# Performance work log

Hardware: AMD Instinct MI355X
Metric: run time of the kernel (lower is better)

The kernel has to match this reference:

```python
import jax, jax.numpy as jnp
import numpy as np

EOS_COEF = 0.1


def setup_inputs() -> dict:
    key = jax.random.key(0)
    k1, k2, k3, k4 = jax.random.split(key, 4)
    B, Q, T, P, M = 8, 256, 128, 100, 512
    pred_patch_logits = jax.random.normal(k1, (B, Q, 2), dtype=jnp.float32)
    pred_patch_points = jax.random.normal(k2, (B, Q, P, 3), dtype=jnp.float32)
    tgt_points = jax.random.normal(k3, (B, T, M, 3), dtype=jnp.float32)
    src_idx = jax.random.randint(k4, (B, T), 0, Q, dtype=jnp.int64)
    return {
        'pred_patch_logits': pred_patch_logits,
        'pred_patch_points': pred_patch_points,
        'tgt_points': tgt_points,
        'src_idx': src_idx,
    }


def reference(pred_patch_logits, pred_patch_points, tgt_points, src_idx):
    B, Q, C = pred_patch_logits.shape
    T = src_idx.shape[1]
    P = pred_patch_points.shape[2]
    M = tgt_points.shape[2]
    N = B * T  # total matched patches = num_patches
    bidx = jnp.arange(B)[:, None]

    # ---- loss_valid_labels (weighted CE, empty_weight = [1, eos_coef]) ----
    w = jnp.array([1.0, EOS_COEF], dtype=pred_patch_logits.dtype)
    target_classes = jnp.ones((B, Q), jnp.int32).at[bidx, src_idx].set(0)
    logp = jax.nn.log_softmax(pred_patch_logits, axis=-1)          # [B,Q,2]
    nll = -jnp.take_along_axis(logp, target_classes[..., None], axis=-1)[..., 0]
    wt = w[target_classes]
    loss_ce = jnp.sum(nll * wt) / jnp.sum(wt)

    # accuracy@1 on matched queries (targets are all class 0) and overall
    matched_logits = pred_patch_logits[bidx, src_idx]              # [B,T,2]
    acc_valid = 100.0 * jnp.mean((jnp.argmax(matched_logits, -1) == 0).astype(jnp.float32))
    acc_overall = 100.0 * jnp.mean((jnp.argmax(pred_patch_logits, -1) == target_classes).astype(jnp.float32))

    # ---- loss_cardinality (no-grad, logging) ----
    card_pred = jnp.sum((jnp.argmax(pred_patch_logits, -1) != (C - 1)).astype(jnp.float32), axis=1)
    card_err = jnp.mean(jnp.abs(card_pred - jnp.float32(T)))

    # ---- loss_geometry: per-patch squared chamfer, fused over all patches ----
    src = pred_patch_points[bidx, src_idx].reshape(N, P, 3)        # matched preds
    tgt = tgt_points.reshape(N, M, 3)
    # squared pairwise distances [N,P,M] = |a|^2 + |b|^2 - 2 a.b
    d2 = (jnp.sum(src * src, -1)[:, :, None]
          + jnp.sum(tgt * tgt, -1)[:, None, :]
          - 2.0 * jnp.einsum('npd,nmd->npm', src, tgt))
    d2 = jnp.maximum(d2, 0.0)
    per_patch = (jnp.mean(jnp.min(d2, axis=1), axis=-1)
                 + 0.2 * jnp.mean(jnp.min(d2, axis=2), axis=-1)) / 1.2  # [N]
    loss_geometry = jnp.sum(per_patch) / jnp.float32(N)

    return (loss_ce, acc_valid, acc_overall, card_err, loss_geometry)
```

## Files before the change

### kernel.cpp

```cpp
#include <hip/hip_runtime.h>
#include <math.h>

#define Bq 8
#define Qq 256
#define Tt 128
#define Pp 100
#define Mm 512
#define Nn 1024

__device__ __forceinline__ float breduce256(float v, float* red) {
    #pragma unroll
    for (int off = 32; off > 0; off >>= 1) v += __shfl_down(v, off, 64);
    __syncthreads();
    if ((threadIdx.x & 63) == 0) red[threadIdx.x >> 6] = v;
    __syncthreads();
    return red[0] + red[1] + red[2] + red[3];
}

__device__ __forceinline__ float dist2(float sx, float sy, float sz, float4 t) {
    const float dx = sx - t.x, dy = sy - t.y, dz = sz - t.z;
    return fmaf(dx, dx, fmaf(dy, dy, dz * dz));
}

__global__ __launch_bounds__(256, 4) void fused_kernel(
    const float* __restrict__ logits,
    const float* __restrict__ pred_pts,
    const float* __restrict__ tgt_pts,
    const int*   __restrict__ src_idx,
    float*       __restrict__ per_patch,
    unsigned*    __restrict__ done_ctr,
    float*       __restrict__ out)
{
    __shared__ float4   s_tgt[Mm];
    __shared__ float4   s_src[128];
    __shared__ unsigned s_amin[Mm];
    __shared__ unsigned s_bmin[128];
    __shared__ float    red[4];
    __shared__ unsigned s_lastflag;
    const int n   = blockIdx.x;
    const int tid = threadIdx.x;
    const int b   = n >> 7;
    const int q   = src_idx[n];
    const float* sp = pred_pts + (size_t)(b * Qq + q) * (Pp * 3);
    const float* tp = tgt_pts  + (size_t)n * (Mm * 3);

    {
        const float2* tp2 = (const float2*)tp;
        const float2 a = tp2[3*tid], c2 = tp2[3*tid+1], e = tp2[3*tid+2];
        s_tgt[2*tid]   = make_float4(a.x, a.y, c2.x, 0.f);
        s_tgt[2*tid+1] = make_float4(c2.y, e.x, e.y, 0.f);
    }
    if (tid < 50) {
        const float2* sp2 = (const float2*)sp;
        const float2 a = sp2[3*tid], c2 = sp2[3*tid+1], e = sp2[3*tid+2];
        s_src[2*tid]   = make_float4(a.x, a.y, c2.x, 0.f);
        s_src[2*tid+1] = make_float4(c2.y, e.x, e.y, 0.f);
    } else if (tid >= 100 && tid < 128) {
        s_src[tid] = make_float4(5e18f, 5e18f, 5e18f, 0.f);
    }
    *(uint2*)&s_amin[2*tid] = make_uint2(0x7f7fffffu, 0x7f7fffffu);
    if (tid < 128) s_bmin[tid] = 0x7f7fffffu;
    __syncthreads();

    const int g     = tid & 15;
    const int c     = tid >> 4;
    const int mbase = c << 5;
    const int rot   = (g + ((c & 3) << 3)) & 31;

    const float4 q0 = s_src[8*g+0], q1 = s_src[8*g+1], q2 = s_src[8*g+2], q3 = s_src[8*g+3];
    const float4 q4 = s_src[8*g+4], q5 = s_src[8*g+5], q6 = s_src[8*g+6], q7 = s_src[8*g+7];
    const float s0x=q0.x, s0y=q0.y, s0z=q0.z;
    const float s1x=q1.x, s1y=q1.y, s1z=q1.z;
    const float s2x=q2.x, s2y=q2.y, s2z=q2.z;
    const float s3x=q3.x, s3y=q3.y, s3z=q3.z;
    const float s4x=q4.x, s4y=q4.y, s4z=q4.z;
    const float s5x=q5.x, s5y=q5.y, s5z=q5.z;
    const float s6x=q6.x, s6y=q6.y, s6z=q6.z;
    const float s7x=q7.x, s7y=q7.y, s7z=q7.z;
    float mn0 = 3.4e38f, mn1 = 3.4e38f, mn2 = 3.4e38f, mn3 = 3.4e38f;
    float mn4 = 3.4e38f, mn5 = 3.4e38f, mn6 = 3.4e38f, mn7 = 3.4e38f;

    #pragma unroll 8
    for (int j = 0; j < 32; ++j) {
        const int m = mbase + ((j + rot) & 31);
        const float4 t = s_tgt[m];
        const float d0 = dist2(s0x,s0y,s0z,t); mn0 = fminf(mn0,d0);
        const float d1 = dist2(s1x,s1y,s1z,t); mn1 = fminf(mn1,d1);
        const float d2 = dist2(s2x,s2y,s2z,t); mn2 = fminf(mn2,d2);
        const float d3 = dist2(s3x,s3y,s3z,t); mn3 = fminf(mn3,d3);
        const float d4 = dist2(s4x,s4y,s4z,t); mn4 = fminf(mn4,d4);
        const float d5 = dist2(s5x,s5y,s5z,t); mn5 = fminf(mn5,d5);
        const float d6 = dist2(s6x,s6y,s6z,t); mn6 = fminf(mn6,d6);
        const float d7 = dist2(s7x,s7y,s7z,t); mn7 = fminf(mn7,d7);
        const float pm = fminf(fminf(fminf(d0,d1), fminf(d2,d3)),
                               fminf(fminf(d4,d5), fminf(d6,d7)));
        atomicMin(&s_amin[m], __float_as_uint(pm));
    }
    atomicMin(&s_bmin[8*g+0], __float_as_uint(mn0));
    atomicMin(&s_bmin[8*g+1], __float_as_uint(mn1));
    atomicMin(&s_bmin[8*g+2], __float_as_uint(mn2));
    atomicMin(&s_bmin[8*g+3], __float_as_uint(mn3));
    atomicMin(&s_bmin[8*g+4], __float_as_uint(mn4));
    atomicMin(&s_bmin[8*g+5], __float_as_uint(mn5));
    atomicMin(&s_bmin[8*g+6], __float_as_uint(mn6));
    atomicMin(&s_bmin[8*g+7], __float_as_uint(mn7));
    __syncthreads();

    float contrib;
    {
        const uint2 u = *(const uint2*)&s_amin[2*tid];
        contrib = (__uint_as_float(u.x) + __uint_as_float(u.y)) * (1.0f / Mm);
    }
    if (tid < Pp) contrib += 0.2f * __uint_as_float(s_bmin[tid]) * (1.0f / Pp);

    const float tot = breduce256(contrib, red);
    if (tid == 0) {
        per_patch[n] = tot * (1.0f / 1.2f);
        __threadfence();
        s_lastflag = (atomicAdd(done_ctr, 1u) == (unsigned)(Nn - 1));
    }
    __syncthreads();
    if (!s_lastflag) return;

    __shared__ unsigned char matched[Bq * Qq];
    __shared__ int s_card[Bq];
    for (int i = tid; i < Bq * Qq; i += 256) matched[i] = 0;
    if (tid < Bq) s_card[tid] = 0;
    __syncthreads();
    for (int i = tid; i < Nn; i += 256) matched[(i >> 7) * Qq + src_idx[i]] = 1;
    __syncthreads();

    float sum_nll = 0.f, sum_wt = 0.f, cnt_ov = 0.f;
    #pragma unroll
    for (int k = 0; k < 8; ++k) {
        const int i = tid + (k << 8);
        const float2 l = ((const float2*)logits)[i];
        const int mt = matched[i];
        const float mx  = fmaxf(l.x, l.y);
        const float lse = mx + logf(expf(l.x - mx) + expf(l.y - mx));
        sum_nll += (mt ? 1.0f : 0.1f) * (lse - (mt ? l.x : l.y));
        sum_wt  += mt ? 1.0f : 0.1f;
        const int pred0 = (l.x >= l.y) ? 1 : 0;
        cnt_ov += (pred0 == mt) ? 1.f : 0.f;
        const unsigned long long bal = __ballot(pred0);
        if ((tid & 63) == 0) atomicAdd(&s_card[k], (int)__popcll(bal));
    }
    float cnt_va = 0.f, gsum = 0.f;
    const volatile float* vpp = per_patch;
    for (int i = tid; i < Nn; i += 256) {
        const float2 l = ((const float2*)logits)[(i >> 7) * Qq + src_idx[i]];
        cnt_va += (l.x >= l.y) ? 1.f : 0.f;
        gsum   += vpp[i];
    }

    const float t_nll = breduce256(sum_nll, red);
    const float t_wt  = breduce256(sum_wt,  red);
    const float t_ov  = breduce256(cnt_ov,  red);
    const float t_va  = breduce256(cnt_va,  red);
    const float t_gs  = breduce256(gsum,    red);

    if (tid == 0) {
        float cerr = 0.f;
        for (int bb = 0; bb < Bq; ++bb) cerr += fabsf((float)s_card[bb] - (float)Tt);
        out[0] = t_nll / t_wt;
        out[1] = 100.f * t_va / (float)Nn;
        out[2] = 100.f * t_ov / (float)(Bq * Qq);
        out[3] = cerr / (float)Bq;
        out[4] = t_gs / (float)Nn;
    }
}

extern "C" void kernel_launch(void* const* d_in, const int* in_sizes, int n_in,
                              void* d_out, int out_size, void* d_ws, size_t ws_size,
                              hipStream_t stream) {
    const float* logits   = (const float*)d_in[0];
    const float* pred_pts = (const float*)d_in[1];
    const float* tgt_pts  = (const float*)d_in[2];
    const int*   src_idx  = (const int*)  d_in[3];
    float* out       = (float*)d_out;
    float* per_patch = (float*)d_ws;
    unsigned* ctr    = (unsigned*)((char*)d_ws + 4096);

    hipMemsetAsync(ctr, 0, sizeof(unsigned), stream);
    fused_kernel<<<Nn, 256, 0, stream>>>(logits, pred_pts, tgt_pts, src_idx,
                                         per_patch, ctr, out);
}
```

Measured before the change: 101.3 us.

## Replace LDS staging and atomics with direct loads and DPP row reductions

Drops the shared-memory staging of target and source points. Each thread now reads its source points directly from global memory as float4 and broadcast-reads target coordinates from global/L1. The per-target minimum over the 16 lanes covering all predicted points is taken with DPP row reductions and summed in registers, which removes the 512 per-target LDS atomics. Per-source minima are reduced with cross-row shuffles before fewer LDS atomics. The 100 points are covered by letting lanes 12-15 duplicate points 92-99, which min tolerates. The risk is slower scalar global loads in the inner loop in place of LDS reads.

```diff
diff --git a/kernel.cpp b/kernel.cpp
--- a/kernel.cpp
+++ b/kernel.cpp
@@ -17,9 +17,17 @@
     return red[0] + red[1] + red[2] + red[3];
 }
 
-__device__ __forceinline__ float dist2(float sx, float sy, float sz, float4 t) {
-    const float dx = sx - t.x, dy = sy - t.y, dz = sz - t.z;
-    return fmaf(dx, dx, fmaf(dy, dy, dz * dz));
+template<int CTRL>
+__device__ __forceinline__ float dpp_min_step(float v) {
+    const int x = __builtin_amdgcn_update_dpp(0, __float_as_int(v), CTRL, 0xF, 0xF, true);
+    return fminf(v, __int_as_float(x));
+}
+__device__ __forceinline__ float row16_min(float v) {
+    v = dpp_min_step<0xB1>(v);
+    v = dpp_min_step<0x4E>(v);
+    v = dpp_min_step<0x124>(v);
+    v = dpp_min_step<0x128>(v);
+    return v;
 }
 
 __global__ __launch_bounds__(256, 4) void fused_kernel(
@@ -31,9 +39,6 @@
     unsigned*    __restrict__ done_ctr,
     float*       __restrict__ out)
 {
-    __shared__ float4   s_tgt[Mm];
-    __shared__ float4   s_src[128];
-    __shared__ unsigned s_amin[Mm];
     __shared__ unsigned s_bmin[128];
     __shared__ float    red[4];
     __shared__ unsigned s_lastflag;
@@ -44,73 +49,81 @@
     const float* sp = pred_pts + (size_t)(b * Qq + q) * (Pp * 3);
     const float* tp = tgt_pts  + (size_t)n * (Mm * 3);
 
-    {
-        const float2* tp2 = (const float2*)tp;
-        const float2 a = tp2[3*tid], c2 = tp2[3*tid+1], e = tp2[3*tid+2];
-        s_tgt[2*tid]   = make_float4(a.x, a.y, c2.x, 0.f);
-        s_tgt[2*tid+1] = make_float4(c2.y, e.x, e.y, 0.f);
-    }
-    if (tid < 50) {
-        const float2* sp2 = (const float2*)sp;
-        const float2 a = sp2[3*tid], c2 = sp2[3*tid+1], e = sp2[3*tid+2];
-        s_src[2*tid]   = make_float4(a.x, a.y, c2.x, 0.f);
-        s_src[2*tid+1] = make_float4(c2.y, e.x, e.y, 0.f);
-    } else if (tid >= 100 && tid < 128) {
-        s_src[tid] = make_float4(5e18f, 5e18f, 5e18f, 0.f);
-    }
-    *(uint2*)&s_amin[2*tid] = make_uint2(0x7f7fffffu, 0x7f7fffffu);
     if (tid < 128) s_bmin[tid] = 0x7f7fffffu;
-    __syncthreads();
 
     const int g     = tid & 15;
-    const int c     = tid >> 4;
-    const int mbase = c << 5;
-    const int rot   = (g + ((c & 3) << 3)) & 31;
-
-    const float4 q0 = s_src[8*g+0], q1 = s_src[8*g+1], q2 = s_src[8*g+2], q3 = s_src[8*g+3];
-    const float4 q4 = s_src[8*g+4], q5 = s_src[8*g+5], q6 = s_src[8*g+6], q7 = s_src[8*g+7];
-    const float s0x=q0.x, s0y=q0.y, s0z=q0.z;
-    const float s1x=q1.x, s1y=q1.y, s1z=q1.z;
-    const float s2x=q2.x, s2y=q2.y, s2z=q2.z;
-    const float s3x=q3.x, s3y=q3.y, s3z=q3.z;
-    const float s4x=q4.x, s4y=q4.y, s4z=q4.z;
-    const float s5x=q5.x, s5y=q5.y, s5z=q5.z;
-    const float s6x=q6.x, s6y=q6.y, s6z=q6.z;
-    const float s7x=q7.x, s7y=q7.y, s7z=q7.z;
+    const int C     = tid >> 4;
+    const int pbase = (g < 12) ? 8 * g : 92;
+
+    const float4* s4 = (const float4*)(sp + pbase * 3);
+    const float4 v0 = s4[0], v1 = s4[1], v2 = s4[2],
+                 v3 = s4[3], v4 = s4[4], v5 = s4[5];
+    float s0x=v0.x, s0y=v0.y, s0z=v0.z;
+    float s1x=v0.w, s1y=v1.x, s1z=v1.y;
+    float s2x=v1.z, s2y=v1.w, s2z=v2.x;
+    float s3x=v2.y, s3y=v2.z, s3z=v2.w;
+    float s4x=v3.x, s4y=v3.y, s4z=v3.z;
+    float s5x=v3.w, s5y=v4.x, s5z=v4.y;
+    float s6x=v4.z, s6y=v4.w, s6z=v5.x;
+    float s7x=v5.y, s7y=v5.z, s7z=v5.w;
+    asm volatile("" : "+v"(s0x),"+v"(s0y),"+v"(s0z),"+v"(s1x),"+v"(s1y),"+v"(s1z),
+                      "+v"(s2x),"+v"(s2y),"+v"(s2z),"+v"(s3x),"+v"(s3y),"+v"(s3z),
+                      "+v"(s4x),"+v"(s4y),"+v"(s4z),"+v"(s5x),"+v"(s5y),"+v"(s5z),
+                      "+v"(s6x),"+v"(s6y),"+v"(s6z),"+v"(s7x),"+v"(s7y),"+v"(s7z));
+
     float mn0 = 3.4e38f, mn1 = 3.4e38f, mn2 = 3.4e38f, mn3 = 3.4e38f;
     float mn4 = 3.4e38f, mn5 = 3.4e38f, mn6 = 3.4e38f, mn7 = 3.4e38f;
-
-    #pragma unroll 8
+    float sumA = 0.f;
+    const float* tbase = tp + C * 96;
+
+    #pragma unroll 4
     for (int j = 0; j < 32; ++j) {
-        const int m = mbase + ((j + rot) & 31);
-        const float4 t = s_tgt[m];
-        const float d0 = dist2(s0x,s0y,s0z,t); mn0 = fminf(mn0,d0);
-        const float d1 = dist2(s1x,s1y,s1z,t); mn1 = fminf(mn1,d1);
-        const float d2 = dist2(s2x,s2y,s2z,t); mn2 = fminf(mn2,d2);
-        const float d3 = dist2(s3x,s3y,s3z,t); mn3 = fminf(mn3,d3);
-        const float d4 = dist2(s4x,s4y,s4z,t); mn4 = fminf(mn4,d4);
-        const float d5 = dist2(s5x,s5y,s5z,t); mn5 = fminf(mn5,d5);
-        const float d6 = dist2(s6x,s6y,s6z,t); mn6 = fminf(mn6,d6);
-        const float d7 = dist2(s7x,s7y,s7z,t); mn7 = fminf(mn7,d7);
-        const float pm = fminf(fminf(fminf(d0,d1), fminf(d2,d3)),
-                               fminf(fminf(d4,d5), fminf(d6,d7)));
-        atomicMin(&s_amin[m], __float_as_uint(pm));
-    }
-    atomicMin(&s_bmin[8*g+0], __float_as_uint(mn0));
-    atomicMin(&s_bmin[8*g+1], __float_as_uint(mn1));
-    atomicMin(&s_bmin[8*g+2], __float_as_uint(mn2));
-    atomicMin(&s_bmin[8*g+3], __float_as_uint(mn3));
-    atomicMin(&s_bmin[8*g+4], __float_as_uint(mn4));
-    atomicMin(&s_bmin[8*g+5], __float_as_uint(mn5));
-    atomicMin(&s_bmin[8*g+6], __float_as_uint(mn6));
-    atomicMin(&s_bmin[8*g+7], __float_as_uint(mn7));
-    __syncthreads();
-
-    float contrib;
-    {
-        const uint2 u = *(const uint2*)&s_amin[2*tid];
-        contrib = (__uint_as_float(u.x) + __uint_as_float(u.y)) * (1.0f / Mm);
-    }
+        const float tx = tbase[3*j+0], ty = tbase[3*j+1], tz = tbase[3*j+2];
+        float dx, dy, dz;
+        dx = s0x-tx; dy = s0y-ty; dz = s0z-tz;
+        const float d0 = fmaf(dx,dx,fmaf(dy,dy,dz*dz)); mn0 = fminf(mn0,d0);
+        dx = s1x-tx; dy = s1y-ty; dz = s1z-tz;
+        const float d1 = fmaf(dx,dx,fmaf(dy,dy,dz*dz)); mn1 = fminf(mn1,d1);
+        dx = s2x-tx; dy = s2y-ty; dz = s2z-tz;
+        const float d2 = fmaf(dx,dx,fmaf(dy,dy,dz*dz)); mn2 = fminf(mn2,d2);
+        dx = s3x-tx; dy = s3y-ty; dz = s3z-tz;
+        const float d3 = fmaf(dx,dx,fmaf(dy,dy,dz*dz)); mn3 = fminf(mn3,d3);
+        dx = s4x-tx; dy = s4y-ty; dz = s4z-tz;
+        const float d4 = fmaf(dx,dx,fmaf(dy,dy,dz*dz)); mn4 = fminf(mn4,d4);
+        dx = s5x-tx; dy = s5y-ty; dz = s5z-tz;
+        const float d5 = fmaf(dx,dx,fmaf(dy,dy,dz*dz)); mn5 = fminf(mn5,d5);
+        dx = s6x-tx; dy = s6y-ty; dz = s6z-tz;
+        const float d6 = fmaf(dx,dx,fmaf(dy,dy,dz*dz)); mn6 = fminf(mn6,d6);
+        dx = s7x-tx; dy = s7y-ty; dz = s7z-tz;
+        const float d7 = fmaf(dx,dx,fmaf(dy,dy,dz*dz)); mn7 = fminf(mn7,d7);
+        float pm = fminf(fminf(fminf(d0,d1), fminf(d2,d3)),
+                         fminf(fminf(d4,d5), fminf(d6,d7)));
+        pm = row16_min(pm);
+        sumA += pm;
+    }
+
+    mn0 = fminf(mn0, __shfl_xor(mn0,16,64)); mn0 = fminf(mn0, __shfl_xor(mn0,32,64));
+    mn1 = fminf(mn1, __shfl_xor(mn1,16,64)); mn1 = fminf(mn1, __shfl_xor(mn1,32,64));
+    mn2 = fminf(mn2, __shfl_xor(mn2,16,64)); mn2 = fminf(mn2, __shfl_xor(mn2,32,64));
+    mn3 = fminf(mn3, __shfl_xor(mn3,16,64)); mn3 = fminf(mn3, __shfl_xor(mn3,32,64));
+    mn4 = fminf(mn4, __shfl_xor(mn4,16,64)); mn4 = fminf(mn4, __shfl_xor(mn4,32,64));
+    mn5 = fminf(mn5, __shfl_xor(mn5,16,64)); mn5 = fminf(mn5, __shfl_xor(mn5,32,64));
+    mn6 = fminf(mn6, __shfl_xor(mn6,16,64)); mn6 = fminf(mn6, __shfl_xor(mn6,32,64));
+    mn7 = fminf(mn7, __shfl_xor(mn7,16,64)); mn7 = fminf(mn7, __shfl_xor(mn7,32,64));
+    __syncthreads();
+    if (((tid >> 4) & 3) == 0) {
+        atomicMin(&s_bmin[pbase+0], __float_as_uint(mn0));
+        atomicMin(&s_bmin[pbase+1], __float_as_uint(mn1));
+        atomicMin(&s_bmin[pbase+2], __float_as_uint(mn2));
+        atomicMin(&s_bmin[pbase+3], __float_as_uint(mn3));
+        atomicMin(&s_bmin[pbase+4], __float_as_uint(mn4));
+        atomicMin(&s_bmin[pbase+5], __float_as_uint(mn5));
+        atomicMin(&s_bmin[pbase+6], __float_as_uint(mn6));
+        atomicMin(&s_bmin[pbase+7], __float_as_uint(mn7));
+    }
+    __syncthreads();
+
+    float contrib = sumA * (1.0f / (16.0f * Mm));
     if (tid < Pp) contrib += 0.2f * __uint_as_float(s_bmin[tid]) * (1.0f / Pp);
 
     const float tot = breduce256(contrib, red);
```

Measured after the change: 106.5 us. +5.1%, slower.
